# Kernel optimization log

Hardware: AMD Instinct MI355X
Metric: run time of the kernel (lower is better)

The kernel has to match this reference:

```python
import jax, jax.numpy as jnp
import numpy as np
import math

FEAT_DIM, M, K = 512, 64, 256
D = FEAT_DIM // M  # 8
ALPHA = 1.0
B = 16384


def setup_inputs() -> dict:
    key = jax.random.key(0)
    kx, kc = jax.random.split(key)
    x = jax.random.normal(kx, (B, FEAT_DIM), dtype=jnp.float32)
    # Codebook: unit-norm codewords scaled by 1/sqrt(M), mimicking the
    # normalized-hypersphere init (orthogonal rotation / permutation do not
    # change the math, only the values).
    c = jax.random.normal(kc, (M, K, D), dtype=jnp.float32)
    c = c / jnp.linalg.norm(c, axis=-1, keepdims=True) / math.sqrt(M)
    return {"x": x, "C": c}


def reference(x, C):
    # x: (B, feat_dim) -> (B, M, D)
    x_ = x.reshape(x.shape[0], M, D)
    # per-subspace inner products with codewords: (B, M, K)
    ips = jnp.einsum('bmd,mkd->bmk', x_, C)
    # training-mode straight-through assignment
    soft = jax.nn.softmax(ips * (M / ALPHA), axis=-1)
    hard = jax.nn.one_hot(jnp.argmax(ips, axis=-1), K, dtype=ips.dtype)
    codes = jax.lax.stop_gradient(hard - soft) + soft
    # reconstruction: (B, M, D) -> (B, feat_dim)
    x_hat = jnp.einsum('mkd,bmk->bmd', C, codes).reshape(x.shape[0], -1)
    return x_hat, codes
```

## Files before the change

kernel.cpp:

```cpp
#include <hip/hip_runtime.h>
#include <math.h>


#define B_SZ   16384
#define FEAT   512
#define M_SZ   64
#define K_SZ   256
#define D_SZ   8

__global__ __launch_bounds__(256) void pq_argmax(
    const float* __restrict__ x,
    const float* __restrict__ C,
    unsigned char* __restrict__ bestk8)
{
#pragma clang fp contract(off)

    const int m     = blockIdx.x & (M_SZ - 1);
    const int chunk = blockIdx.x >> 6;
    const int b     = (chunk << 8) | threadIdx.x;

    const float* xp = x + (size_t)b * FEAT + m * D_SZ;
    const float4 xa = *(const float4*)(xp);
    const float4 xb = *(const float4*)(xp + 4);

    const float* __restrict__ Cm = C + (size_t)m * (K_SZ * D_SZ);

    float best  = -INFINITY;
    int   bestk = 0;

#pragma unroll 8
    for (int k = 0; k < K_SZ; ++k) {
        const float* cr = Cm + k * D_SZ;
        float s0 = xa.x * cr[0];
        float s1 = xa.y * cr[1];
        float s2 = xa.z * cr[2];
        float s3 = xa.w * cr[3];
        float s4 = xb.x * cr[4];
        float s5 = xb.y * cr[5];
        float s6 = xb.z * cr[6];
        float s7 = xb.w * cr[7];
        float t0 = s0 + s4;
        float t1 = s1 + s5;
        float t2 = s2 + s6;
        float t3 = s3 + s7;
        float dot = (t0 + t1) + (t2 + t3);
        if (dot > best) { best = dot; bestk = k; }
    }

    bestk8[(size_t)m * B_SZ + b] = (unsigned char)bestk;
}

__global__ __launch_bounds__(256) void pq_write(
    const float* __restrict__ C,
    const unsigned char* __restrict__ bestk8,
    float* __restrict__ xhat,
    float* __restrict__ codes)
{
    const int t    = threadIdx.x;
    const int b0   = blockIdx.x << 2;
    const int r    = t >> 6;
    const int lane = t & 63;
    const int b    = b0 + r;

    const int kb = (int)bestk8[(size_t)lane * B_SZ + b];

    {
        const float* cw = C + ((size_t)lane * K_SZ + kb) * D_SZ;
        const float4 h0 = ((const float4*)cw)[0];
        const float4 h1 = ((const float4*)cw)[1];
        float* xh = xhat + (size_t)b * FEAT + lane * D_SZ;
        ((float4*)xh)[0] = h0;
        ((float4*)xh)[1] = h1;
    }

    {
        const float4 z = {0.f, 0.f, 0.f, 0.f};
        float4* slab = (float4*)(codes + (size_t)b0 * (M_SZ * K_SZ));
#pragma unroll 8
        for (int i = t; i < 16384; i += 256) slab[i] = z;
    }

    __syncthreads();

    codes[((size_t)b * M_SZ + lane) * K_SZ + kb] = 1.0f;
}

extern "C" void kernel_launch(void* const* d_in, const int* in_sizes, int n_in,
                              void* d_out, int out_size, void* d_ws, size_t ws_size,
                              hipStream_t stream)
{
    const float* x = (const float*)d_in[0];
    const float* C = (const float*)d_in[1];
    float* xhat  = (float*)d_out;
    float* codes = (float*)d_out + (size_t)B_SZ * FEAT;
    unsigned char* bestk8 = (unsigned char*)d_ws;

    hipLaunchKernelGGL(pq_argmax, dim3(4096), dim3(256), 0, stream, x, C, bestk8);
    hipLaunchKernelGGL(pq_write,  dim3(4096), dim3(256), 0, stream, C, bestk8, xhat, codes);
}
```

Measured before the change: 1.256 ms.

## Write one-hot codes in a single pass and transpose bestk index layout

```diff
diff --git a/kernel.cpp b/kernel.cpp
--- a/kernel.cpp
+++ b/kernel.cpp
@@ -15,13 +15,16 @@
 {
 #pragma clang fp contract(off)
 
-    const int m     = blockIdx.x & (M_SZ - 1);
-    const int chunk = blockIdx.x >> 6;
-    const int b     = (chunk << 8) | threadIdx.x;
+    const int idx  = blockIdx.x;
+    const int g    = ((idx >> 5) << 3) | (idx & 7);
+    const int mm   = (idx >> 3) & 3;
+    const int m    = ((g & 15) << 2) | mm;
+    const int chunk = g >> 4;
+    const int b    = (chunk << 8) | threadIdx.x;
 
     const float* xp = x + (size_t)b * FEAT + m * D_SZ;
-    const float4 xa = *(const float4*)(xp);
-    const float4 xb = *(const float4*)(xp + 4);
+    const float4 xa = ((const float4*)xp)[0];
+    const float4 xb = ((const float4*)xp)[1];
 
     const float* __restrict__ Cm = C + (size_t)m * (K_SZ * D_SZ);
 
@@ -47,10 +50,10 @@
         if (dot > best) { best = dot; bestk = k; }
     }
 
-    bestk8[(size_t)m * B_SZ + b] = (unsigned char)bestk;
+    bestk8[(size_t)b * M_SZ + m] = (unsigned char)bestk;
 }
 
-__global__ __launch_bounds__(256) void pq_write(
+__global__ __launch_bounds__(256) void pq_fill(
     const float* __restrict__ C,
     const unsigned char* __restrict__ bestk8,
     float* __restrict__ xhat,
@@ -58,13 +61,16 @@
 {
     const int t    = threadIdx.x;
     const int b0   = blockIdx.x << 2;
-    const int r    = t >> 6;
+    const int w    = t >> 6;
     const int lane = t & 63;
-    const int b    = b0 + r;
 
-    const int kb = (int)bestk8[(size_t)lane * B_SZ + b];
+    __shared__ unsigned char lbk[4 * M_SZ];
+
+    lbk[t] = bestk8[(size_t)b0 * M_SZ + t];
 
     {
+        const int b  = b0 + w;
+        const int kb = (int)bestk8[(size_t)b * M_SZ + lane];
         const float* cw = C + ((size_t)lane * K_SZ + kb) * D_SZ;
         const float4 h0 = ((const float4*)cw)[0];
         const float4 h1 = ((const float4*)cw)[1];
@@ -73,16 +79,23 @@
         ((float4*)xh)[1] = h1;
     }
 
-    {
-        const float4 z = {0.f, 0.f, 0.f, 0.f};
-        float4* slab = (float4*)(codes + (size_t)b0 * (M_SZ * K_SZ));
-#pragma unroll 8
-        for (int i = t; i < 16384; i += 256) slab[i] = z;
-    }
-
     __syncthreads();
 
-    codes[((size_t)b * M_SZ + lane) * K_SZ + kb] = 1.0f;
+    const int lane4 = lane << 2;
+    float4* const slab = (float4*)(codes + (size_t)b0 * (M_SZ * K_SZ));
+
+#pragma unroll 4
+    for (int j = 0; j < 64; ++j) {
+        const int r  = j >> 4;
+        const int mj = (w + 4 * j) & 63;
+        const int kk = (int)lbk[(r << 6) | mj];
+        float4 v;
+        v.x = (kk == lane4 + 0) ? 1.0f : 0.0f;
+        v.y = (kk == lane4 + 1) ? 1.0f : 0.0f;
+        v.z = (kk == lane4 + 2) ? 1.0f : 0.0f;
+        v.w = (kk == lane4 + 3) ? 1.0f : 0.0f;
+        slab[t + 256 * j] = v;
+    }
 }
 
 extern "C" void kernel_launch(void* const* d_in, const int* in_sizes, int n_in,
@@ -96,5 +109,5 @@
     unsigned char* bestk8 = (unsigned char*)d_ws;
 
     hipLaunchKernelGGL(pq_argmax, dim3(4096), dim3(256), 0, stream, x, C, bestk8);
-    hipLaunchKernelGGL(pq_write,  dim3(4096), dim3(256), 0, stream, C, bestk8, xhat, codes);
+    hipLaunchKernelGGL(pq_fill,   dim3(4096), dim3(256), 0, stream, C, bestk8, xhat, codes);
 }
```

Result: faster. 1.205 ms (-4.1%).
